# Optimization experiments

Hardware: AMD Instinct MI355X
Metric: run time of the kernel (lower is better)

The kernel has to match this reference:

```python
import jax, jax.numpy as jnp
import numpy as np

D_K = 512  # module-level global used for the scale factor


def setup_inputs() -> dict:
    key = jax.random.key(0)
    kq, kk, kv, km = jax.random.split(key, 4)
    B, H, L = 4, 8, 1024
    Q = jax.random.normal(kq, (B, H, L, D_K), dtype=jnp.float32)
    K = jax.random.normal(kk, (B, H, L, D_K), dtype=jnp.float32)
    V = jax.random.normal(kv, (B, H, L, D_K), dtype=jnp.float32)
    attn_mask = jax.random.randint(km, (B, H, L, L), 0, 2).astype(jnp.bool_)
    return {"Q": Q, "K": K, "V": V, "attn_mask": attn_mask}


def reference(Q, K, V, attn_mask):
    scale = 1.0 / np.sqrt(D_K).astype(np.float32)
    # [B,H,Lq,Lk]
    scores = jnp.einsum('bhqd,bhkd->bhqk', Q, K) * scale
    scores = jnp.where(attn_mask, jnp.float32(-1e9), scores)
    attn = jax.nn.softmax(scores, axis=-1)
    context = jnp.einsum('bhqk,bhkd->bhqd', attn, V)
    return (context, attn)
```

## Files before the change

### kernel.cpp

```cpp
#include <hip/hip_runtime.h>
#include <hip/hip_bf16.h>

constexpr int BH  = 32;
constexpr int LQ  = 1024;
constexpr int DK  = 512;
constexpr float SCALE = 0.04419417382415922f;

using short8 = __attribute__((ext_vector_type(8))) short;
using f32x4  = __attribute__((ext_vector_type(4))) float;

__device__ __forceinline__ unsigned short cvt_bf16(float x) {
  unsigned int u = __builtin_bit_cast(unsigned int, x);
  u += 0x7FFFu + ((u >> 16) & 1u);
  return (unsigned short)(u >> 16);
}
__device__ __forceinline__ float bf2f(unsigned short s) {
  return __builtin_bit_cast(float, (unsigned int)s << 16);
}
__device__ __forceinline__ unsigned int pack2(float a, float b) {
  return (unsigned int)cvt_bf16(a) | ((unsigned int)cvt_bf16(b) << 16);
}

__device__ __forceinline__ void lds_load16(const void* g, void* l) {
  __builtin_amdgcn_global_load_lds(
      (const __attribute__((address_space(1))) unsigned int*)g,
      (__attribute__((address_space(3))) unsigned int*)l, 16, 0, 0);
}

__global__ __launch_bounds__(256) void cvt2_f32_bf16(
    const float* __restrict__ s0, const float* __restrict__ s1,
    unsigned short* __restrict__ d0, unsigned short* __restrict__ d1, int n8) {
  const float* src = blockIdx.y ? s1 : s0;
  unsigned short* dst = blockIdx.y ? d1 : d0;
  int i = blockIdx.x * 256 + threadIdx.x;
  const int stride = gridDim.x * 256;
  for (; i < n8; i += stride) {
    float4 a = ((const float4*)src)[(size_t)i * 2];
    float4 b = ((const float4*)src)[(size_t)i * 2 + 1];
    unsigned short us[8] __attribute__((aligned(16)));
    us[0]=cvt_bf16(a.x); us[1]=cvt_bf16(a.y); us[2]=cvt_bf16(a.z); us[3]=cvt_bf16(a.w);
    us[4]=cvt_bf16(b.x); us[5]=cvt_bf16(b.y); us[6]=cvt_bf16(b.z); us[7]=cvt_bf16(b.w);
    ((short8*)dst)[i] = *(short8*)us;
  }
}

__global__ __launch_bounds__(256) void qk_exp_kernel(
    const unsigned short* __restrict__ A, const unsigned short* __restrict__ B,
    const int* __restrict__ mask, unsigned short* __restrict__ P,
    float* __restrict__ partials) {
  __shared__ __attribute__((aligned(16))) unsigned short smem[32768];

  int flat = blockIdx.x + 8 * (blockIdx.y + 8 * blockIdx.z);
  flat = (flat % 8) * 256 + flat / 8;
  const int bx = flat % 8;
  const int by = (flat / 8) % 8;
  const int bh = flat / 64;

  const int t = threadIdx.x;
  const int lane = t & 63, wave = t >> 6;
  const int wr = wave >> 1, wc = wave & 1;
  const int fr = lane & 15, fq = lane >> 4;
  const int m0 = by * 128, n0 = bx * 128;

  const char* Ab = (const char*)A + ((size_t)bh * LQ + m0) * 1024;
  const char* Bb = (const char*)B + ((size_t)bh * LQ + n0) * 1024;

  unsigned int orv = 0;
  {
    const unsigned int* mw = (const unsigned int*)mask;
    #pragma unroll
    for (int i = 0; i < 64; ++i) orv |= mw[i];
  }
  const bool byteMode = (orv > 1u);

  f32x4 acc[4][4];
  #pragma unroll
  for (int i = 0; i < 4; ++i)
    #pragma unroll
    for (int j = 0; j < 4; ++j) acc[i][j] = (f32x4){0.f, 0.f, 0.f, 0.f};

  auto STAGE = [&](int kb, int buf) {
    char* base = (char*)smem + buf * 32768;
    #pragma unroll
    for (int i = 0; i < 4; ++i) {
      const int p  = i * 4096 + t * 16;
      const int r  = p >> 7;
      const int ch = (p >> 4) & 7;
      const int sw = ((ch ^ (r & 7)) << 4);
      lds_load16(Ab + (size_t)r * 1024 + kb + sw, base + wave * 1024 + i * 4096);
      lds_load16(Bb + (size_t)r * 1024 + kb + sw, base + 16384 + wave * 1024 + i * 4096);
    }
  };
  auto COMPUTE = [&](int buf) {
    const char* As = (const char*)smem + buf * 32768;
    const char* Bs = As + 16384;
    #pragma unroll
    for (int kk = 0; kk < 2; ++kk) {
      short8 a[4], b[4];
      #pragma unroll
      for (int mi = 0; mi < 4; ++mi) {
        const int r  = wr * 64 + mi * 16 + fr;
        const int ch = (kk * 4 + fq) ^ (r & 7);
        a[mi] = *(const short8*)(As + r * 128 + ch * 16);
      }
      #pragma unroll
      for (int ni = 0; ni < 4; ++ni) {
        const int r  = wc * 64 + ni * 16 + fr;
        const int ch = (kk * 4 + fq) ^ (r & 7);
        b[ni] = *(const short8*)(Bs + r * 128 + ch * 16);
      }
      #pragma unroll
      for (int mi = 0; mi < 4; ++mi)
        #pragma unroll
        for (int ni = 0; ni < 4; ++ni)
          acc[mi][ni] = __builtin_amdgcn_mfma_f32_16x16x32_bf16(a[mi], b[ni], acc[mi][ni], 0, 0, 0);
    }
  };

  STAGE(0, 0);
  __syncthreads();
  int cur = 0;
  for (int it = 0; it < 8; ++it) {
    if (it < 7) STAGE((it + 1) * 128, cur ^ 1);
    COMPUTE(cur);
    __syncthreads();
    cur ^= 1;
  }

  unsigned short* Cs = smem;
  #pragma unroll
  for (int mi = 0; mi < 4; ++mi)
    #pragma unroll
    for (int ni = 0; ni < 4; ++ni) {
      const int col = wc * 64 + ni * 16 + fr;
      #pragma unroll
      for (int r = 0; r < 4; ++r) {
        const int row = wr * 64 + mi * 16 + fq * 4 + r;
        Cs[row * 128 + col] = cvt_bf16(__expf(acc[mi][ni][r] * SCALE));
      }
    }
  __syncthreads();

  const int rl = t >> 4;
  const int cl = (t & 15) * 8;
  const size_t pbase = (size_t)bh * LQ * LQ;
  #pragma unroll
  for (int rb = 0; rb < 8; ++rb) {
    const int rloc = rb * 16 + rl;
    const int rg   = m0 + rloc;
    const size_t gidx = pbase + (size_t)rg * LQ + (n0 + cl);
    short8 sv = *(const short8*)&Cs[rloc * 128 + cl];
    bool mk[8];
    if (byteMode) {
      const unsigned char* mb = (const unsigned char*)mask + gidx;
      uint2 w = *(const uint2*)mb;
      #pragma unroll
      for (int j = 0; j < 4; ++j) mk[j]     = ((w.x >> (8 * j)) & 255u) != 0u;
      #pragma unroll
      for (int j = 0; j < 4; ++j) mk[4 + j] = ((w.y >> (8 * j)) & 255u) != 0u;
    } else {
      int4 w0 = *(const int4*)(mask + gidx);
      int4 w1 = *(const int4*)(mask + gidx + 4);
      mk[0] = w0.x != 0; mk[1] = w0.y != 0; mk[2] = w0.z != 0; mk[3] = w0.w != 0;
      mk[4] = w1.x != 0; mk[5] = w1.y != 0; mk[6] = w1.z != 0; mk[7] = w1.w != 0;
    }
    unsigned short out[8] __attribute__((aligned(16)));
    float s = 0.f;
    #pragma unroll
    for (int j = 0; j < 8; ++j) {
      unsigned short v = mk[j] ? (unsigned short)0 : (unsigned short)sv[j];
      out[j] = v;
      s += bf2f(v);
    }
    *(short8*)(P + gidx) = *(short8*)out;
    s += __shfl_xor(s, 1); s += __shfl_xor(s, 2);
    s += __shfl_xor(s, 4); s += __shfl_xor(s, 8);
    if ((t & 15) == 0)
      partials[((size_t)bh * LQ + rg) * 8 + bx] = s;
  }
}

__global__ __launch_bounds__(256) void attn_fin(
    const unsigned short* __restrict__ P, const float* __restrict__ partials,
    float* __restrict__ attn) {
  const int ch = blockIdx.x, rb64 = blockIdx.y, bh = blockIdx.z;
  const int m0 = rb64 * 64;
  __shared__ float invs[64];
  const int t = threadIdx.x;
  if (t < 64) {
    const float* pp = partials + ((size_t)bh * LQ + m0 + t) * 8;
    float s = ((pp[0] + pp[1]) + (pp[2] + pp[3])) + ((pp[4] + pp[5]) + (pp[6] + pp[7]));
    invs[t] = 1.0f / s;
  }
  __syncthreads();
  const size_t pbase = (size_t)bh * LQ * LQ;
  const int c0 = ch * 512;
  #pragma unroll
  for (int rb = 0; rb < 4; ++rb) {
    const int rloc = rb * 16 + (t >> 4);
    const int row  = m0 + rloc;
    const float inv = invs[rloc];
    const size_t base = pbase + (size_t)row * LQ + c0 + (t & 15) * 8;
    #pragma unroll
    for (int j = 0; j < 4; ++j) {
      short8 sv = *(const short8*)(P + base + j * 128);
      float4 o0, o1;
      o0.x = bf2f((unsigned short)sv[0]) * inv;
      o0.y = bf2f((unsigned short)sv[1]) * inv;
      o0.z = bf2f((unsigned short)sv[2]) * inv;
      o0.w = bf2f((unsigned short)sv[3]) * inv;
      o1.x = bf2f((unsigned short)sv[4]) * inv;
      o1.y = bf2f((unsigned short)sv[5]) * inv;
      o1.z = bf2f((unsigned short)sv[6]) * inv;
      o1.w = bf2f((unsigned short)sv[7]) * inv;
      *(float4*)(attn + base + j * 128)     = o0;
      *(float4*)(attn + base + j * 128 + 4) = o1;
    }
  }
}

__global__ __launch_bounds__(256) void pv2_kernel(
    const unsigned short* __restrict__ P, const float* __restrict__ V,
    const float* __restrict__ partials, float* __restrict__ O) {
  __shared__ __attribute__((aligned(16))) unsigned short As[8192];
  __shared__ __attribute__((aligned(16))) unsigned short BsV[128 * 72];
  __shared__ float invsL[128];

  int flat = blockIdx.x + 4 * (blockIdx.y + 8 * blockIdx.z);
  flat = (flat % 8) * 128 + flat / 8;
  const int bx = flat % 4;
  const int by = (flat / 4) % 8;
  const int bh = flat / 32;

  const int t = threadIdx.x;
  const int lane = t & 63, wave = t >> 6;
  const int wr = wave >> 1, wc = wave & 1;
  const int fr = lane & 15, fq = lane >> 4;
  const int m0 = by * 128, n0 = bx * 128;

  if (t < 128) {
    const float* pp = partials + ((size_t)bh * LQ + m0 + t) * 8;
    float s = ((pp[0] + pp[1]) + (pp[2] + pp[3])) + ((pp[4] + pp[5]) + (pp[6] + pp[7]));
    invsL[t] = 1.0f / s;
  }

  const char* Ab  = (const char*)P + ((size_t)bh * LQ + m0) * 2048;
  const float* Vb = V + (size_t)bh * LQ * DK + n0;

  f32x4 acc[4][4];
  #pragma unroll
  for (int i = 0; i < 4; ++i)
    #pragma unroll
    for (int j = 0; j < 4; ++j) acc[i][j] = (f32x4){0.f, 0.f, 0.f, 0.f};

  const int g  = t >> 5;
  const int nl = t & 31;

  for (int k0 = 0; k0 < LQ; k0 += 64) {
    __syncthreads();
    #pragma unroll
    for (int i = 0; i < 4; ++i) {
      const int p  = i * 4096 + t * 16;
      const int r  = p >> 7;
      const int ch = (p >> 4) & 7;
      const int sw = ((ch ^ (r & 7)) << 4);
      lds_load16(Ab + (size_t)r * 2048 + k0 * 2 + sw, (char*)As + wave * 1024 + i * 4096);
    }
    float vf[8][4];
    #pragma unroll
    for (int i = 0; i < 8; ++i) {
      const size_t rb = (size_t)(k0 + 8 * g + i) * DK;
      #pragma unroll
      for (int jn = 0; jn < 4; ++jn)
        vf[i][jn] = Vb[rb + nl + 32 * jn];
    }
    #pragma unroll
    for (int jn = 0; jn < 4; ++jn) {
      const int n = nl + 32 * jn;
      uint2 w0, w1;
      w0.x = pack2(vf[0][jn], vf[1][jn]); w0.y = pack2(vf[2][jn], vf[3][jn]);
      w1.x = pack2(vf[4][jn], vf[5][jn]); w1.y = pack2(vf[6][jn], vf[7][jn]);
      *(uint2*)((char*)BsV + n * 144 + 16 * g)     = w0;
      *(uint2*)((char*)BsV + n * 144 + 16 * g + 8) = w1;
    }
    __syncthreads();

    #pragma unroll
    for (int kk = 0; kk < 2; ++kk) {
      short8 a[4], b[4];
      #pragma unroll
      for (int mi = 0; mi < 4; ++mi) {
        const int r  = wr * 64 + mi * 16 + fr;
        const int ch = (kk * 4 + fq) ^ (r & 7);
        a[mi] = *(const short8*)((const char*)As + r * 128 + ch * 16);
      }
      #pragma unroll
      for (int ni = 0; ni < 4; ++ni) {
        const int r = wc * 64 + ni * 16 + fr;
        b[ni] = *(const short8*)((const char*)BsV + r * 144 + (kk * 4 + fq) * 16);
      }
      #pragma unroll
      for (int mi = 0; mi < 4; ++mi)
        #pragma unroll
        for (int ni = 0; ni < 4; ++ni)
          acc[mi][ni] = __builtin_amdgcn_mfma_f32_16x16x32_bf16(a[mi], b[ni], acc[mi][ni], 0, 0, 0);
    }
  }

  const size_t obase = (size_t)bh * LQ * DK;
  #pragma unroll
  for (int mi = 0; mi < 4; ++mi)
    #pragma unroll
    for (int ni = 0; ni < 4; ++ni) {
      const int col = n0 + wc * 64 + ni * 16 + fr;
      #pragma unroll
      for (int r = 0; r < 4; ++r) {
        const int rloc = wr * 64 + mi * 16 + fq * 4 + r;
        O[obase + (size_t)(m0 + rloc) * DK + col] = acc[mi][ni][r] * invsL[rloc];
      }
    }
}

__global__ __launch_bounds__(256) void qk_mask_kernel(
    const float* __restrict__ Q, const float* __restrict__ Kmat,
    const int* __restrict__ mask, float* __restrict__ S) {
  __shared__ __attribute__((aligned(16))) unsigned short Asf[128][40];
  __shared__ __attribute__((aligned(16))) unsigned short Bsf[128][40];
  const int t = threadIdx.x;
  const int lane = t & 63, wave = t >> 6;
  const int wr = wave >> 1, wc = wave & 1;
  const int fr = lane & 15, fq = lane >> 4;
  const int bh = blockIdx.z;
  const int m0 = blockIdx.y * 128, n0 = blockIdx.x * 128;
  const float* Qb = Q + (size_t)bh * LQ * DK;
  const float* Kb = Kmat + (size_t)bh * LQ * DK;
  unsigned int orv = 0;
  { const unsigned int* mw = (const unsigned int*)mask;
    #pragma unroll
    for (int i = 0; i < 64; ++i) orv |= mw[i]; }
  const bool byteMode = (orv > 1u);
  f32x4 acc[4][4];
  #pragma unroll
  for (int i = 0; i < 4; ++i)
    #pragma unroll
    for (int j = 0; j < 4; ++j) acc[i][j] = (f32x4){0.f,0.f,0.f,0.f};
  const int sr = t >> 1, sc = (t & 1) * 16;
  for (int kd = 0; kd < DK; kd += 32) {
    __syncthreads();
    { const float4* qa = (const float4*)(Qb + (size_t)(m0+sr)*DK + kd + sc);
      float fv[16];
      #pragma unroll
      for (int i = 0; i < 4; ++i) { float4 x = qa[i];
        fv[4*i]=x.x; fv[4*i+1]=x.y; fv[4*i+2]=x.z; fv[4*i+3]=x.w; }
      unsigned short us[16] __attribute__((aligned(16)));
      #pragma unroll
      for (int i = 0; i < 16; ++i) us[i] = cvt_bf16(fv[i]);
      *(short8*)&Asf[sr][sc]   = *(short8*)&us[0];
      *(short8*)&Asf[sr][sc+8] = *(short8*)&us[8]; }
    { const float4* ka = (const float4*)(Kb + (size_t)(n0+sr)*DK + kd + sc);
      float fv[16];
      #pragma unroll
      for (int i = 0; i < 4; ++i) { float4 x = ka[i];
        fv[4*i]=x.x; fv[4*i+1]=x.y; fv[4*i+2]=x.z; fv[4*i+3]=x.w; }
      unsigned short us[16] __attribute__((aligned(16)));
      #pragma unroll
      for (int i = 0; i < 16; ++i) us[i] = cvt_bf16(fv[i]);
      *(short8*)&Bsf[sr][sc]   = *(short8*)&us[0];
      *(short8*)&Bsf[sr][sc+8] = *(short8*)&us[8]; }
    __syncthreads();
    short8 a[4], b[4];
    #pragma unroll
    for (int mi = 0; mi < 4; ++mi) a[mi] = *(const short8*)&Asf[wr*64+mi*16+fr][fq*8];
    #pragma unroll
    for (int ni = 0; ni < 4; ++ni) b[ni] = *(const short8*)&Bsf[wc*64+ni*16+fr][fq*8];
    #pragma unroll
    for (int mi = 0; mi < 4; ++mi)
      #pragma unroll
      for (int ni = 0; ni < 4; ++ni)
        acc[mi][ni] = __builtin_amdgcn_mfma_f32_16x16x32_bf16(a[mi], b[ni], acc[mi][ni], 0, 0, 0);
  }
  const size_t sbase = (size_t)bh * LQ * LQ;
  const unsigned char* mb = (const unsigned char*)mask;
  #pragma unroll
  for (int mi = 0; mi < 4; ++mi)
    #pragma unroll
    for (int ni = 0; ni < 4; ++ni) {
      const int col = n0 + wc*64 + ni*16 + fr;
      #pragma unroll
      for (int r = 0; r < 4; ++r) {
        const int row = m0 + wr*64 + mi*16 + fq*4 + r;
        const size_t idx = sbase + (size_t)row * LQ + col;
        float s = acc[mi][ni][r] * SCALE;
        const bool msk = byteMode ? (mb[idx] != 0) : (mask[idx] != 0);
        S[idx] = msk ? -1e9f : s;
      }
    }
}

__global__ __launch_bounds__(256) void softmax_kernel(float* __restrict__ A) {
  const int row = blockIdx.x;
  float4* rp = (float4*)(A + (size_t)row * LQ);
  const int t = threadIdx.x;
  float4 v = rp[t];
  float m = fmaxf(fmaxf(v.x, v.y), fmaxf(v.z, v.w));
  #pragma unroll
  for (int off = 32; off >= 1; off >>= 1) m = fmaxf(m, __shfl_xor(m, off, 64));
  __shared__ float redm[4];
  const int wv = t >> 6, ln = t & 63;
  if (ln == 0) redm[wv] = m;
  __syncthreads();
  m = fmaxf(fmaxf(redm[0], redm[1]), fmaxf(redm[2], redm[3]));
  float4 e;
  e.x = expf(v.x - m); e.y = expf(v.y - m); e.z = expf(v.z - m); e.w = expf(v.w - m);
  float s = (e.x + e.y) + (e.z + e.w);
  #pragma unroll
  for (int off = 32; off >= 1; off >>= 1) s += __shfl_xor(s, off, 64);
  __shared__ float reds2[4];
  if (ln == 0) reds2[wv] = s;
  __syncthreads();
  s = (reds2[0] + reds2[1]) + (reds2[2] + reds2[3]);
  const float inv = 1.0f / s;
  e.x *= inv; e.y *= inv; e.z *= inv; e.w *= inv;
  rp[t] = e;
}

__global__ __launch_bounds__(256) void pv_kernel(
    const float* __restrict__ P, const float* __restrict__ V, float* __restrict__ O) {
  __shared__ __attribute__((aligned(16))) unsigned short Ps[128][40];
  __shared__ __attribute__((aligned(16))) unsigned short Vtl[128][40];
  const int t = threadIdx.x;
  const int lane = t & 63, wave = t >> 6;
  const int wr = wave >> 1, wc = wave & 1;
  const int fr = lane & 15, fq = lane >> 4;
  const int bh = blockIdx.z;
  const int m0 = blockIdx.y * 128, n0 = blockIdx.x * 128;
  const float* Pb = P + (size_t)bh * LQ * LQ;
  const float* Vb = V + (size_t)bh * LQ * DK;
  f32x4 acc[4][4];
  #pragma unroll
  for (int i = 0; i < 4; ++i)
    #pragma unroll
    for (int j = 0; j < 4; ++j) acc[i][j] = (f32x4){0.f,0.f,0.f,0.f};
  const int sr = t >> 1, sc = (t & 1) * 16;
  const int kk = (t & 15) * 2, nn = (t >> 4) * 8;
  for (int k0 = 0; k0 < LQ; k0 += 32) {
    __syncthreads();
    { const float4* pa = (const float4*)(Pb + (size_t)(m0+sr)*LQ + k0 + sc);
      float fv[16];
      #pragma unroll
      for (int i = 0; i < 4; ++i) { float4 x = pa[i];
        fv[4*i]=x.x; fv[4*i+1]=x.y; fv[4*i+2]=x.z; fv[4*i+3]=x.w; }
      unsigned short us[16] __attribute__((aligned(16)));
      #pragma unroll
      for (int i = 0; i < 16; ++i) us[i] = cvt_bf16(fv[i]);
      *(short8*)&Ps[sr][sc]   = *(short8*)&us[0];
      *(short8*)&Ps[sr][sc+8] = *(short8*)&us[8]; }
    { const float* v0p = Vb + (size_t)(k0+kk)*DK + n0 + nn;
      const float* v1p = v0p + DK;
      float4 a0 = *(const float4*)v0p, a1 = *(const float4*)(v0p+4);
      float4 b0 = *(const float4*)v1p, b1 = *(const float4*)(v1p+4);
      float r0[8] = {a0.x,a0.y,a0.z,a0.w,a1.x,a1.y,a1.z,a1.w};
      float r1[8] = {b0.x,b0.y,b0.z,b0.w,b1.x,b1.y,b1.z,b1.w};
      #pragma unroll
      for (int i = 0; i < 8; ++i) {
        unsigned int pk = (unsigned int)cvt_bf16(r0[i]) | ((unsigned int)cvt_bf16(r1[i]) << 16);
        *(unsigned int*)&Vtl[nn+i][kk] = pk; } }
    __syncthreads();
    short8 a[4], b[4];
    #pragma unroll
    for (int mi = 0; mi < 4; ++mi) a[mi] = *(const short8*)&Ps[wr*64+mi*16+fr][fq*8];
    #pragma unroll
    for (int ni = 0; ni < 4; ++ni) b[ni] = *(const short8*)&Vtl[wc*64+ni*16+fr][fq*8];
    #pragma unroll
    for (int mi = 0; mi < 4; ++mi)
      #pragma unroll
      for (int ni = 0; ni < 4; ++ni)
        acc[mi][ni] = __builtin_amdgcn_mfma_f32_16x16x32_bf16(a[mi], b[ni], acc[mi][ni], 0, 0, 0);
  }
  const size_t obase = (size_t)bh * LQ * DK;
  #pragma unroll
  for (int mi = 0; mi < 4; ++mi)
    #pragma unroll
    for (int ni = 0; ni < 4; ++ni) {
      const int col = n0 + wc*64 + ni*16 + fr;
      #pragma unroll
      for (int r = 0; r < 4; ++r) {
        const int row = m0 + wr*64 + mi*16 + fq*4 + r;
        O[obase + (size_t)row * DK + col] = acc[mi][ni][r];
      }
    }
}

extern "C" void kernel_launch(void* const* d_in, const int* in_sizes, int n_in,
                              void* d_out, int out_size, void* d_ws, size_t ws_size,
                              hipStream_t stream) {
  const float* Q    = (const float*)d_in[0];
  const float* K    = (const float*)d_in[1];
  const float* V    = (const float*)d_in[2];
  const int*   mask = (const int*)d_in[3];

  float* ctx  = (float*)d_out;
  float* attn = ctx + (size_t)BH * LQ * DK;

  const size_t NE = (size_t)BH * LQ * DK;
  const size_t P_BYTES  = (size_t)BH * LQ * LQ * 2;
  const size_t WS_NEED  = P_BYTES + (size_t)BH * LQ * 8 * 4;

  if (ws_size >= WS_NEED) {
    unsigned short* Pp       = (unsigned short*)d_ws;
    float*          partials = (float*)((char*)d_ws + P_BYTES);
    unsigned short* Qb = (unsigned short*)ctx;
    unsigned short* Kb = Qb + NE;

    cvt2_f32_bf16<<<dim3(1024, 2), 256, 0, stream>>>(Q, K, Qb, Kb, (int)(NE / 8));
    qk_exp_kernel<<<dim3(8, 8, BH), 256, 0, stream>>>(Qb, Kb, mask, Pp, partials);
    attn_fin<<<dim3(2, 16, BH), 256, 0, stream>>>(Pp, partials, attn);
    pv2_kernel<<<dim3(4, 8, BH), 256, 0, stream>>>(Pp, V, partials, ctx);
  } else {
    qk_mask_kernel<<<dim3(8, 8, BH), 256, 0, stream>>>(Q, K, mask, attn);
    softmax_kernel<<<dim3(BH * LQ), 256, 0, stream>>>(attn);
    pv_kernel<<<dim3(4, 8, BH), 256, 0, stream>>>(attn, V, ctx);
  }
}
```

Baseline: 237.0 us.

## Enlarge QK tiles to 256x256 with an eight-wave ping-pong MFMA schedule

```diff
diff --git a/kernel.cpp b/kernel.cpp
--- a/kernel.cpp
+++ b/kernel.cpp
@@ -25,6 +25,12 @@
   __builtin_amdgcn_global_load_lds(
       (const __attribute__((address_space(1))) unsigned int*)g,
       (__attribute__((address_space(3))) unsigned int*)l, 16, 0, 0);
+}
+
+__device__ __forceinline__ void barrier_raw() {
+  asm volatile("" ::: "memory");
+  __builtin_amdgcn_s_barrier();
+  asm volatile("" ::: "memory");
 }
 
 __global__ __launch_bounds__(256) void cvt2_f32_bf16(
@@ -44,23 +50,24 @@
   }
 }
 
-__global__ __launch_bounds__(256) void qk_exp_kernel(
+__global__ __launch_bounds__(512, 2) void qk_exp256_kernel(
     const unsigned short* __restrict__ A, const unsigned short* __restrict__ B,
     const int* __restrict__ mask, unsigned short* __restrict__ P,
     float* __restrict__ partials) {
-  __shared__ __attribute__((aligned(16))) unsigned short smem[32768];
-
-  int flat = blockIdx.x + 8 * (blockIdx.y + 8 * blockIdx.z);
-  flat = (flat % 8) * 256 + flat / 8;
-  const int bx = flat % 8;
-  const int by = (flat / 8) % 8;
-  const int bh = flat / 64;
+  __shared__ __attribute__((aligned(16))) unsigned short smem[67584];
+
+  int flat = blockIdx.x + 4 * (blockIdx.y + 4 * blockIdx.z);
+  flat = (flat % 8) * 64 + flat / 8;
+  const int bx = flat % 4;
+  const int by = (flat / 4) % 4;
+  const int bh = flat / 16;
 
   const int t = threadIdx.x;
   const int lane = t & 63, wave = t >> 6;
-  const int wr = wave >> 1, wc = wave & 1;
+  const int wr = wave >> 2;
+  const int wc = wave & 3;
   const int fr = lane & 15, fq = lane >> 4;
-  const int m0 = by * 128, n0 = bx * 128;
+  const int m0 = by * 256, n0 = bx * 256;
 
   const char* Ab = (const char*)A + ((size_t)bh * LQ + m0) * 1024;
   const char* Bb = (const char*)B + ((size_t)bh * LQ + n0) * 1024;
@@ -73,83 +80,135 @@
   }
   const bool byteMode = (orv > 1u);
 
-  f32x4 acc[4][4];
-  #pragma unroll
-  for (int i = 0; i < 4; ++i)
+  f32x4 acc[8][4];
+  #pragma unroll
+  for (int i = 0; i < 8; ++i)
     #pragma unroll
     for (int j = 0; j < 4; ++j) acc[i][j] = (f32x4){0.f, 0.f, 0.f, 0.f};
 
-  auto STAGE = [&](int kb, int buf) {
-    char* base = (char*)smem + buf * 32768;
-    #pragma unroll
-    for (int i = 0; i < 4; ++i) {
-      const int p  = i * 4096 + t * 16;
+  short8 a[4][2], bA[2][2], bB[2][2];
+
+  auto STAGE_A = [&](int tau, int h) {
+    char* dst = (char*)smem + (tau & 1) * 32768 + h * 16384 + wave * 1024;
+    const char* src = Ab + tau * 128;
+    #pragma unroll
+    for (int i = 0; i < 2; ++i) {
+      const int p  = i * 8192 + t * 16;
       const int r  = p >> 7;
       const int ch = (p >> 4) & 7;
-      const int sw = ((ch ^ (r & 7)) << 4);
-      lds_load16(Ab + (size_t)r * 1024 + kb + sw, base + wave * 1024 + i * 4096);
-      lds_load16(Bb + (size_t)r * 1024 + kb + sw, base + 16384 + wave * 1024 + i * 4096);
+      lds_load16(src + (size_t)(h * 128 + r) * 1024 + ((ch ^ (r & 7)) << 4),
+                 dst + i * 8192);
     }
   };
-  auto COMPUTE = [&](int buf) {
-    const char* As = (const char*)smem + buf * 32768;
-    const char* Bs = As + 16384;
-    #pragma unroll
-    for (int kk = 0; kk < 2; ++kk) {
-      short8 a[4], b[4];
-      #pragma unroll
-      for (int mi = 0; mi < 4; ++mi) {
-        const int r  = wr * 64 + mi * 16 + fr;
+  auto STAGE_B = [&](int tau, int h) {
+    char* dst = (char*)smem + 65536 + (tau & 1) * 32768 + h * 16384 + wave * 1024;
+    const char* src = Bb + tau * 128;
+    #pragma unroll
+    for (int i = 0; i < 2; ++i) {
+      const int p  = i * 8192 + t * 16;
+      const int r  = p >> 7;
+      const int ch = (p >> 4) & 7;
+      lds_load16(src + (size_t)(h * 128 + r) * 1024 + ((ch ^ (r & 7)) << 4),
+                 dst + i * 8192);
+    }
+  };
+
+  auto LDA_ = [&](int s, int mh) {
+    const char* As = (const char*)smem + s * 32768;
+    #pragma unroll
+    for (int mi = 0; mi < 4; ++mi)
+      #pragma unroll
+      for (int kk = 0; kk < 2; ++kk) {
+        const int r  = wr * 128 + mh * 64 + mi * 16 + fr;
         const int ch = (kk * 4 + fq) ^ (r & 7);
-        a[mi] = *(const short8*)(As + r * 128 + ch * 16);
-      }
-      #pragma unroll
-      for (int ni = 0; ni < 4; ++ni) {
-        const int r  = wc * 64 + ni * 16 + fr;
+        a[mi][kk] = *(const short8*)(As + r * 128 + ch * 16);
+      }
+  };
+  auto LDB_ = [&](short8 (&b)[2][2], int s, int np) {
+    const char* Bs = (const char*)smem + 65536 + s * 32768;
+    #pragma unroll
+    for (int nj = 0; nj < 2; ++nj)
+      #pragma unroll
+      for (int kk = 0; kk < 2; ++kk) {
+        const int r  = wc * 64 + np * 32 + nj * 16 + fr;
         const int ch = (kk * 4 + fq) ^ (r & 7);
-        b[ni] = *(const short8*)(Bs + r * 128 + ch * 16);
-      }
-      #pragma unroll
-      for (int mi = 0; mi < 4; ++mi)
+        b[nj][kk] = *(const short8*)(Bs + r * 128 + ch * 16);
+      }
+  };
+  auto MMA_ = [&](short8 (&b)[2][2], int mh, int np) {
+    __builtin_amdgcn_s_setprio(1);
+    #pragma unroll
+    for (int mi = 0; mi < 4; ++mi)
+      #pragma unroll
+      for (int nj = 0; nj < 2; ++nj)
         #pragma unroll
-        for (int ni = 0; ni < 4; ++ni)
-          acc[mi][ni] = __builtin_amdgcn_mfma_f32_16x16x32_bf16(a[mi], b[ni], acc[mi][ni], 0, 0, 0);
-    }
+        for (int kk = 0; kk < 2; ++kk)
+          acc[mh * 4 + mi][np * 2 + nj] = __builtin_amdgcn_mfma_f32_16x16x32_bf16(
+              a[mi][kk], b[nj][kk], acc[mh * 4 + mi][np * 2 + nj], 0, 0, 0);
+    __builtin_amdgcn_s_setprio(0);
   };
 
-  STAGE(0, 0);
+  STAGE_A(0, 0); STAGE_A(0, 1);
+  STAGE_B(0, 0); STAGE_B(0, 1);
+  STAGE_B(1, 0); STAGE_B(1, 1);
+  asm volatile("s_waitcnt vmcnt(4)" ::: "memory");
+  barrier_raw();
+
+  for (int kt = 0; kt < 8; kt += 2) {
+    const bool pf = (kt < 6);
+    LDA_(0, 0); LDB_(bA, 0, 0);
+    STAGE_A(kt + 1, 0);
+    barrier_raw(); MMA_(bA, 0, 0); barrier_raw();
+    LDB_(bB, 0, 1);
+    STAGE_A(kt + 1, 1);
+    barrier_raw(); MMA_(bB, 0, 1); barrier_raw();
+    LDA_(0, 1);
+    if (pf) STAGE_B(kt + 2, 0);
+    barrier_raw(); MMA_(bA, 1, 0); barrier_raw();
+    if (pf) STAGE_B(kt + 2, 1);
+    barrier_raw(); MMA_(bB, 1, 1);
+    if (pf) asm volatile("s_waitcnt vmcnt(4)" ::: "memory");
+    else    asm volatile("s_waitcnt vmcnt(0)" ::: "memory");
+    barrier_raw();
+    LDA_(1, 0); LDB_(bA, 1, 0);
+    if (pf) STAGE_A(kt + 2, 0);
+    barrier_raw(); MMA_(bA, 0, 0); barrier_raw();
+    LDB_(bB, 1, 1);
+    if (pf) STAGE_A(kt + 2, 1);
+    barrier_raw(); MMA_(bB, 0, 1); barrier_raw();
+    LDA_(1, 1);
+    if (pf) STAGE_B(kt + 3, 0);
+    barrier_raw(); MMA_(bA, 1, 0); barrier_raw();
+    if (pf) STAGE_B(kt + 3, 1);
+    barrier_raw(); MMA_(bB, 1, 1);
+    if (pf) asm volatile("s_waitcnt vmcnt(4)" ::: "memory");
+    barrier_raw();
+  }
+
   __syncthreads();
-  int cur = 0;
-  for (int it = 0; it < 8; ++it) {
-    if (it < 7) STAGE((it + 1) * 128, cur ^ 1);
-    COMPUTE(cur);
-    __syncthreads();
-    cur ^= 1;
-  }
-
   unsigned short* Cs = smem;
   #pragma unroll
-  for (int mi = 0; mi < 4; ++mi)
+  for (int mi = 0; mi < 8; ++mi)
     #pragma unroll
     for (int ni = 0; ni < 4; ++ni) {
       const int col = wc * 64 + ni * 16 + fr;
       #pragma unroll
       for (int r = 0; r < 4; ++r) {
-        const int row = wr * 64 + mi * 16 + fq * 4 + r;
-        Cs[row * 128 + col] = cvt_bf16(__expf(acc[mi][ni][r] * SCALE));
+        const int row = wr * 128 + mi * 16 + fq * 4 + r;
+        Cs[row * 264 + col] = cvt_bf16(__expf(acc[mi][ni][r] * SCALE));
       }
     }
   __syncthreads();
 
-  const int rl = t >> 4;
-  const int cl = (t & 15) * 8;
+  const int rl = t >> 5;
+  const int cl = (t & 31) * 8;
   const size_t pbase = (size_t)bh * LQ * LQ;
   #pragma unroll
-  for (int rb = 0; rb < 8; ++rb) {
+  for (int rb = 0; rb < 16; ++rb) {
     const int rloc = rb * 16 + rl;
     const int rg   = m0 + rloc;
     const size_t gidx = pbase + (size_t)rg * LQ + (n0 + cl);
-    short8 sv = *(const short8*)&Cs[rloc * 128 + cl];
+    short8 sv = *(const short8*)&Cs[rloc * 264 + cl];
     bool mk[8];
     if (byteMode) {
       const unsigned char* mb = (const unsigned char*)mask + gidx;
@@ -173,10 +232,10 @@
       s += bf2f(v);
     }
     *(short8*)(P + gidx) = *(short8*)out;
-    s += __shfl_xor(s, 1); s += __shfl_xor(s, 2);
-    s += __shfl_xor(s, 4); s += __shfl_xor(s, 8);
-    if ((t & 15) == 0)
-      partials[((size_t)bh * LQ + rg) * 8 + bx] = s;
+    s += __shfl_xor(s, 1);  s += __shfl_xor(s, 2);
+    s += __shfl_xor(s, 4);  s += __shfl_xor(s, 8);  s += __shfl_xor(s, 16);
+    if ((t & 31) == 0)
+      partials[((size_t)bh * LQ + rg) * 4 + bx] = s;
   }
 }
 
@@ -188,8 +247,8 @@
   __shared__ float invs[64];
   const int t = threadIdx.x;
   if (t < 64) {
-    const float* pp = partials + ((size_t)bh * LQ + m0 + t) * 8;
-    float s = ((pp[0] + pp[1]) + (pp[2] + pp[3])) + ((pp[4] + pp[5]) + (pp[6] + pp[7]));
+    const float* pp = partials + ((size_t)bh * LQ + m0 + t) * 4;
+    float s = (pp[0] + pp[1]) + (pp[2] + pp[3]);
     invs[t] = 1.0f / s;
   }
   __syncthreads();
@@ -239,8 +298,8 @@
   const int m0 = by * 128, n0 = bx * 128;
 
   if (t < 128) {
-    const float* pp = partials + ((size_t)bh * LQ + m0 + t) * 8;
-    float s = ((pp[0] + pp[1]) + (pp[2] + pp[3])) + ((pp[4] + pp[5]) + (pp[6] + pp[7]));
+    const float* pp = partials + ((size_t)bh * LQ + m0 + t) * 4;
+    float s = (pp[0] + pp[1]) + (pp[2] + pp[3]);
     invsL[t] = 1.0f / s;
   }
 
@@ -504,7 +563,7 @@
 
   const size_t NE = (size_t)BH * LQ * DK;
   const size_t P_BYTES  = (size_t)BH * LQ * LQ * 2;
-  const size_t WS_NEED  = P_BYTES + (size_t)BH * LQ * 8 * 4;
+  const size_t WS_NEED  = P_BYTES + (size_t)BH * LQ * 4 * 4;
 
   if (ws_size >= WS_NEED) {
     unsigned short* Pp       = (unsigned short*)d_ws;
@@ -513,7 +572,7 @@
     unsigned short* Kb = Qb + NE;
 
     cvt2_f32_bf16<<<dim3(1024, 2), 256, 0, stream>>>(Q, K, Qb, Kb, (int)(NE / 8));
-    qk_exp_kernel<<<dim3(8, 8, BH), 256, 0, stream>>>(Qb, Kb, mask, Pp, partials);
+    qk_exp256_kernel<<<dim3(4, 4, BH), 512, 0, stream>>>(Qb, Kb, mask, Pp, partials);
     attn_fin<<<dim3(2, 16, BH), 256, 0, stream>>>(Pp, partials, attn);
     pv2_kernel<<<dim3(4, 8, BH), 256, 0, stream>>>(Pp, V, partials, ctx);
   } else {
```

Measured after the change: 236.8 us. No clear change (-0.1%).

## Fuse attention normalization into PV kernel and enlarge QK tile to 256 rows

Applied to the files above, without the earlier changes.

```diff
diff --git a/kernel.cpp b/kernel.cpp
--- a/kernel.cpp
+++ b/kernel.cpp
@@ -44,17 +44,160 @@
   }
 }
 
-__global__ __launch_bounds__(256) void qk_exp_kernel(
+__global__ __launch_bounds__(512) void qk_v4_kernel(
     const unsigned short* __restrict__ A, const unsigned short* __restrict__ B,
     const int* __restrict__ mask, unsigned short* __restrict__ P,
     float* __restrict__ partials) {
-  __shared__ __attribute__((aligned(16))) unsigned short smem[32768];
-
-  int flat = blockIdx.x + 8 * (blockIdx.y + 8 * blockIdx.z);
-  flat = (flat % 8) * 256 + flat / 8;
+  __shared__ __attribute__((aligned(16))) unsigned short smem[24576];
+
+  int flat = blockIdx.x + 8 * (blockIdx.y + 4 * blockIdx.z);
+  flat = (flat % 8) * 128 + flat / 8;
   const int bx = flat % 8;
-  const int by = (flat / 8) % 8;
-  const int bh = flat / 64;
+  const int by = (flat / 8) % 4;
+  const int bh = flat / 32;
+
+  const int t = threadIdx.x;
+  const int lane = t & 63, wave = t >> 6;
+  const int wr = wave >> 1;
+  const int wc = wave & 1;
+  const int fr = lane & 15, fq = lane >> 4;
+  const int m0 = by * 256, n0 = bx * 128;
+
+  const char* Ab = (const char*)A + ((size_t)bh * LQ + m0) * 1024;
+  const char* Bb = (const char*)B + ((size_t)bh * LQ + n0) * 1024;
+
+  unsigned int orv = 0;
+  {
+    const unsigned int* mw = (const unsigned int*)mask;
+    #pragma unroll
+    for (int i = 0; i < 64; ++i) orv |= mw[i];
+  }
+  const bool byteMode = (orv > 1u);
+
+  f32x4 acc[4][4];
+  #pragma unroll
+  for (int i = 0; i < 4; ++i)
+    #pragma unroll
+    for (int j = 0; j < 4; ++j) acc[i][j] = (f32x4){0.f, 0.f, 0.f, 0.f};
+
+  char* const AsB = (char*)smem;
+  char* const BsB = (char*)smem + 32768;
+
+  for (int kt = 0; kt < 8; ++kt) {
+    const int kb = kt * 128;
+    __syncthreads();
+    #pragma unroll
+    for (int i = 0; i < 4; ++i) {
+      const int p  = i * 8192 + t * 16;
+      const int r  = p >> 7;
+      const int ch = (p >> 4) & 7;
+      lds_load16(Ab + (size_t)r * 1024 + kb + ((ch ^ (r & 7)) << 4),
+                 AsB + i * 8192 + wave * 1024);
+    }
+    #pragma unroll
+    for (int i = 0; i < 2; ++i) {
+      const int p  = i * 8192 + t * 16;
+      const int r  = p >> 7;
+      const int ch = (p >> 4) & 7;
+      lds_load16(Bb + (size_t)r * 1024 + kb + ((ch ^ (r & 7)) << 4),
+                 BsB + i * 8192 + wave * 1024);
+    }
+    __syncthreads();
+
+    #pragma unroll
+    for (int kk = 0; kk < 2; ++kk) {
+      short8 a[4], b[4];
+      #pragma unroll
+      for (int mi = 0; mi < 4; ++mi) {
+        const int r  = wr * 64 + mi * 16 + fr;
+        const int ch = (kk * 4 + fq) ^ (r & 7);
+        a[mi] = *(const short8*)(AsB + r * 128 + ch * 16);
+      }
+      #pragma unroll
+      for (int ni = 0; ni < 4; ++ni) {
+        const int r  = wc * 64 + ni * 16 + fr;
+        const int ch = (kk * 4 + fq) ^ (r & 7);
+        b[ni] = *(const short8*)(BsB + r * 128 + ch * 16);
+      }
+      #pragma unroll
+      for (int mi = 0; mi < 4; ++mi)
+        #pragma unroll
+        for (int ni = 0; ni < 4; ++ni)
+          acc[mi][ni] = __builtin_amdgcn_mfma_f32_16x16x32_bf16(a[mi], b[ni], acc[mi][ni], 0, 0, 0);
+    }
+  }
+
+  unsigned short* Cs = smem;
+  const size_t pbase = (size_t)bh * LQ * LQ;
+  #pragma unroll
+  for (int h = 0; h < 2; ++h) {
+    __syncthreads();
+    if ((wr >> 1) == h) {
+      #pragma unroll
+      for (int mi = 0; mi < 4; ++mi)
+        #pragma unroll
+        for (int ni = 0; ni < 4; ++ni) {
+          const int col = wc * 64 + ni * 16 + fr;
+          #pragma unroll
+          for (int r = 0; r < 4; ++r) {
+            const int rloc = (wr & 1) * 64 + mi * 16 + fq * 4 + r;
+            Cs[rloc * 136 + col] = cvt_bf16(__expf(acc[mi][ni][r] * SCALE));
+          }
+        }
+    }
+    __syncthreads();
+    const int rl = t >> 4;
+    const int cl = (t & 15) * 8;
+    #pragma unroll
+    for (int rb = 0; rb < 4; ++rb) {
+      const int rloc = rb * 32 + rl;
+      const int rg   = m0 + h * 128 + rloc;
+      const size_t gidx = pbase + (size_t)rg * LQ + (n0 + cl);
+      short8 sv = *(const short8*)&Cs[rloc * 136 + cl];
+      bool mk[8];
+      if (byteMode) {
+        const unsigned char* mb = (const unsigned char*)mask + gidx;
+        uint2 w = *(const uint2*)mb;
+        #pragma unroll
+        for (int j = 0; j < 4; ++j) mk[j]     = ((w.x >> (8 * j)) & 255u) != 0u;
+        #pragma unroll
+        for (int j = 0; j < 4; ++j) mk[4 + j] = ((w.y >> (8 * j)) & 255u) != 0u;
+      } else {
+        int4 w0 = *(const int4*)(mask + gidx);
+        int4 w1 = *(const int4*)(mask + gidx + 4);
+        mk[0] = w0.x != 0; mk[1] = w0.y != 0; mk[2] = w0.z != 0; mk[3] = w0.w != 0;
+        mk[4] = w1.x != 0; mk[5] = w1.y != 0; mk[6] = w1.z != 0; mk[7] = w1.w != 0;
+      }
+      unsigned short out[8] __attribute__((aligned(16)));
+      float s = 0.f;
+      #pragma unroll
+      for (int j = 0; j < 8; ++j) {
+        unsigned short v = mk[j] ? (unsigned short)0 : (unsigned short)sv[j];
+        out[j] = v;
+        s += bf2f(v);
+      }
+      *(short8*)(P + gidx) = *(short8*)out;
+      s += __shfl_xor(s, 1); s += __shfl_xor(s, 2);
+      s += __shfl_xor(s, 4); s += __shfl_xor(s, 8);
+      if ((t & 15) == 0)
+        partials[((size_t)bh * LQ + rg) * 8 + bx] = s;
+    }
+  }
+}
+
+__global__ __launch_bounds__(256) void pv2f_kernel(
+    const unsigned short* __restrict__ P, const float* __restrict__ V,
+    const float* __restrict__ partials, float* __restrict__ O,
+    float* __restrict__ attn) {
+  __shared__ __attribute__((aligned(16))) unsigned short As[8192];
+  __shared__ __attribute__((aligned(16))) unsigned short BsV[128 * 72];
+  __shared__ float invsL[128];
+
+  int flat = blockIdx.x + 4 * (blockIdx.y + 8 * blockIdx.z);
+  flat = (flat % 8) * 128 + flat / 8;
+  const int bx = flat % 4;
+  const int by = (flat / 4) % 8;
+  const int bh = flat / 32;
 
   const int t = threadIdx.x;
   const int lane = t & 63, wave = t >> 6;
@@ -62,182 +205,6 @@
   const int fr = lane & 15, fq = lane >> 4;
   const int m0 = by * 128, n0 = bx * 128;
 
-  const char* Ab = (const char*)A + ((size_t)bh * LQ + m0) * 1024;
-  const char* Bb = (const char*)B + ((size_t)bh * LQ + n0) * 1024;
-
-  unsigned int orv = 0;
-  {
-    const unsigned int* mw = (const unsigned int*)mask;
-    #pragma unroll
-    for (int i = 0; i < 64; ++i) orv |= mw[i];
-  }
-  const bool byteMode = (orv > 1u);
-
-  f32x4 acc[4][4];
-  #pragma unroll
-  for (int i = 0; i < 4; ++i)
-    #pragma unroll
-    for (int j = 0; j < 4; ++j) acc[i][j] = (f32x4){0.f, 0.f, 0.f, 0.f};
-
-  auto STAGE = [&](int kb, int buf) {
-    char* base = (char*)smem + buf * 32768;
-    #pragma unroll
-    for (int i = 0; i < 4; ++i) {
-      const int p  = i * 4096 + t * 16;
-      const int r  = p >> 7;
-      const int ch = (p >> 4) & 7;
-      const int sw = ((ch ^ (r & 7)) << 4);
-      lds_load16(Ab + (size_t)r * 1024 + kb + sw, base + wave * 1024 + i * 4096);
-      lds_load16(Bb + (size_t)r * 1024 + kb + sw, base + 16384 + wave * 1024 + i * 4096);
-    }
-  };
-  auto COMPUTE = [&](int buf) {
-    const char* As = (const char*)smem + buf * 32768;
-    const char* Bs = As + 16384;
-    #pragma unroll
-    for (int kk = 0; kk < 2; ++kk) {
-      short8 a[4], b[4];
-      #pragma unroll
-      for (int mi = 0; mi < 4; ++mi) {
-        const int r  = wr * 64 + mi * 16 + fr;
-        const int ch = (kk * 4 + fq) ^ (r & 7);
-        a[mi] = *(const short8*)(As + r * 128 + ch * 16);
-      }
-      #pragma unroll
-      for (int ni = 0; ni < 4; ++ni) {
-        const int r  = wc * 64 + ni * 16 + fr;
-        const int ch = (kk * 4 + fq) ^ (r & 7);
-        b[ni] = *(const short8*)(Bs + r * 128 + ch * 16);
-      }
-      #pragma unroll
-      for (int mi = 0; mi < 4; ++mi)
-        #pragma unroll
-        for (int ni = 0; ni < 4; ++ni)
-          acc[mi][ni] = __builtin_amdgcn_mfma_f32_16x16x32_bf16(a[mi], b[ni], acc[mi][ni], 0, 0, 0);
-    }
-  };
-
-  STAGE(0, 0);
-  __syncthreads();
-  int cur = 0;
-  for (int it = 0; it < 8; ++it) {
-    if (it < 7) STAGE((it + 1) * 128, cur ^ 1);
-    COMPUTE(cur);
-    __syncthreads();
-    cur ^= 1;
-  }
-
-  unsigned short* Cs = smem;
-  #pragma unroll
-  for (int mi = 0; mi < 4; ++mi)
-    #pragma unroll
-    for (int ni = 0; ni < 4; ++ni) {
-      const int col = wc * 64 + ni * 16 + fr;
-      #pragma unroll
-      for (int r = 0; r < 4; ++r) {
-        const int row = wr * 64 + mi * 16 + fq * 4 + r;
-        Cs[row * 128 + col] = cvt_bf16(__expf(acc[mi][ni][r] * SCALE));
-      }
-    }
-  __syncthreads();
-
-  const int rl = t >> 4;
-  const int cl = (t & 15) * 8;
-  const size_t pbase = (size_t)bh * LQ * LQ;
-  #pragma unroll
-  for (int rb = 0; rb < 8; ++rb) {
-    const int rloc = rb * 16 + rl;
-    const int rg   = m0 + rloc;
-    const size_t gidx = pbase + (size_t)rg * LQ + (n0 + cl);
-    short8 sv = *(const short8*)&Cs[rloc * 128 + cl];
-    bool mk[8];
-    if (byteMode) {
-      const unsigned char* mb = (const unsigned char*)mask + gidx;
-      uint2 w = *(const uint2*)mb;
-      #pragma unroll
-      for (int j = 0; j < 4; ++j) mk[j]     = ((w.x >> (8 * j)) & 255u) != 0u;
-      #pragma unroll
-      for (int j = 0; j < 4; ++j) mk[4 + j] = ((w.y >> (8 * j)) & 255u) != 0u;
-    } else {
-      int4 w0 = *(const int4*)(mask + gidx);
-      int4 w1 = *(const int4*)(mask + gidx + 4);
-      mk[0] = w0.x != 0; mk[1] = w0.y != 0; mk[2] = w0.z != 0; mk[3] = w0.w != 0;
-      mk[4] = w1.x != 0; mk[5] = w1.y != 0; mk[6] = w1.z != 0; mk[7] = w1.w != 0;
-    }
-    unsigned short out[8] __attribute__((aligned(16)));
-    float s = 0.f;
-    #pragma unroll
-    for (int j = 0; j < 8; ++j) {
-      unsigned short v = mk[j] ? (unsigned short)0 : (unsigned short)sv[j];
-      out[j] = v;
-      s += bf2f(v);
-    }
-    *(short8*)(P + gidx) = *(short8*)out;
-    s += __shfl_xor(s, 1); s += __shfl_xor(s, 2);
-    s += __shfl_xor(s, 4); s += __shfl_xor(s, 8);
-    if ((t & 15) == 0)
-      partials[((size_t)bh * LQ + rg) * 8 + bx] = s;
-  }
-}
-
-__global__ __launch_bounds__(256) void attn_fin(
-    const unsigned short* __restrict__ P, const float* __restrict__ partials,
-    float* __restrict__ attn) {
-  const int ch = blockIdx.x, rb64 = blockIdx.y, bh = blockIdx.z;
-  const int m0 = rb64 * 64;
-  __shared__ float invs[64];
-  const int t = threadIdx.x;
-  if (t < 64) {
-    const float* pp = partials + ((size_t)bh * LQ + m0 + t) * 8;
-    float s = ((pp[0] + pp[1]) + (pp[2] + pp[3])) + ((pp[4] + pp[5]) + (pp[6] + pp[7]));
-    invs[t] = 1.0f / s;
-  }
-  __syncthreads();
-  const size_t pbase = (size_t)bh * LQ * LQ;
-  const int c0 = ch * 512;
-  #pragma unroll
-  for (int rb = 0; rb < 4; ++rb) {
-    const int rloc = rb * 16 + (t >> 4);
-    const int row  = m0 + rloc;
-    const float inv = invs[rloc];
-    const size_t base = pbase + (size_t)row * LQ + c0 + (t & 15) * 8;
-    #pragma unroll
-    for (int j = 0; j < 4; ++j) {
-      short8 sv = *(const short8*)(P + base + j * 128);
-      float4 o0, o1;
-      o0.x = bf2f((unsigned short)sv[0]) * inv;
-      o0.y = bf2f((unsigned short)sv[1]) * inv;
-      o0.z = bf2f((unsigned short)sv[2]) * inv;
-      o0.w = bf2f((unsigned short)sv[3]) * inv;
-      o1.x = bf2f((unsigned short)sv[4]) * inv;
-      o1.y = bf2f((unsigned short)sv[5]) * inv;
-      o1.z = bf2f((unsigned short)sv[6]) * inv;
-      o1.w = bf2f((unsigned short)sv[7]) * inv;
-      *(float4*)(attn + base + j * 128)     = o0;
-      *(float4*)(attn + base + j * 128 + 4) = o1;
-    }
-  }
-}
-
-__global__ __launch_bounds__(256) void pv2_kernel(
-    const unsigned short* __restrict__ P, const float* __restrict__ V,
-    const float* __restrict__ partials, float* __restrict__ O) {
-  __shared__ __attribute__((aligned(16))) unsigned short As[8192];
-  __shared__ __attribute__((aligned(16))) unsigned short BsV[128 * 72];
-  __shared__ float invsL[128];
-
-  int flat = blockIdx.x + 4 * (blockIdx.y + 8 * blockIdx.z);
-  flat = (flat % 8) * 128 + flat / 8;
-  const int bx = flat % 4;
-  const int by = (flat / 4) % 8;
-  const int bh = flat / 32;
-
-  const int t = threadIdx.x;
-  const int lane = t & 63, wave = t >> 6;
-  const int wr = wave >> 1, wc = wave & 1;
-  const int fr = lane & 15, fq = lane >> 4;
-  const int m0 = by * 128, n0 = bx * 128;
-
   if (t < 128) {
     const float* pp = partials + ((size_t)bh * LQ + m0 + t) * 8;
     float s = ((pp[0] + pp[1]) + (pp[2] + pp[3])) + ((pp[4] + pp[5]) + (pp[6] + pp[7]));
@@ -246,6 +213,7 @@
 
   const char* Ab  = (const char*)P + ((size_t)bh * LQ + m0) * 2048;
   const float* Vb = V + (size_t)bh * LQ * DK + n0;
+  float* attnB = attn + ((size_t)bh * LQ + m0) * LQ;
 
   f32x4 acc[4][4];
   #pragma unroll
@@ -284,6 +252,28 @@
       *(uint2*)((char*)BsV + n * 144 + 16 * g + 8) = w1;
     }
     __syncthreads();
+
+    if ((k0 >> 8) == bx) {
+      #pragma unroll
+      for (int rep = 0; rep < 4; ++rep) {
+        const int r  = rep * 32 + (t >> 3);
+        const int ch = t & 7;
+        short8 sv = *(const short8*)((const char*)As + r * 128 + ((ch ^ (r & 7)) << 4));
+        const float inv = invsL[r];
+        float4 o0, o1;
+        o0.x = bf2f((unsigned short)sv[0]) * inv;
+        o0.y = bf2f((unsigned short)sv[1]) * inv;
+        o0.z = bf2f((unsigned short)sv[2]) * inv;
+        o0.w = bf2f((unsigned short)sv[3]) * inv;
+        o1.x = bf2f((unsigned short)sv[4]) * inv;
+        o1.y = bf2f((unsigned short)sv[5]) * inv;
+        o1.z = bf2f((unsigned short)sv[6]) * inv;
+        o1.w = bf2f((unsigned short)sv[7]) * inv;
+        float* dst = attnB + (size_t)r * LQ + k0 + ch * 8;
+        *(float4*)dst       = o0;
+        *(float4*)(dst + 4) = o1;
+      }
+    }
 
     #pragma unroll
     for (int kk = 0; kk < 2; ++kk) {
@@ -513,9 +503,8 @@
     unsigned short* Kb = Qb + NE;
 
     cvt2_f32_bf16<<<dim3(1024, 2), 256, 0, stream>>>(Q, K, Qb, Kb, (int)(NE / 8));
-    qk_exp_kernel<<<dim3(8, 8, BH), 256, 0, stream>>>(Qb, Kb, mask, Pp, partials);
-    attn_fin<<<dim3(2, 16, BH), 256, 0, stream>>>(Pp, partials, attn);
-    pv2_kernel<<<dim3(4, 8, BH), 256, 0, stream>>>(Pp, V, partials, ctx);
+    qk_v4_kernel<<<dim3(8, 4, BH), 512, 0, stream>>>(Qb, Kb, mask, Pp, partials);
+    pv2f_kernel<<<dim3(4, 8, BH), 256, 0, stream>>>(Pp, V, partials, ctx, attn);
   } else {
     qk_mask_kernel<<<dim3(8, 8, BH), 256, 0, stream>>>(Q, K, mask, attn);
     softmax_kernel<<<dim3(BH * LQ), 256, 0, stream>>>(attn);
```

After: 224.0 us. 1.06x faster.
